# Optimization experiments

Measured on AMD Instinct MI355X. Metric: run time of the kernel, lower is better.

The kernel has to match this reference:

```python
import jax, jax.numpy as jnp
import numpy as np

N, D, H = 2048, 64, 64  # num_nodes, in_channels, hidden_channels


def setup_inputs() -> dict:
    key = jax.random.key(0)
    k0, k1, k2 = jax.random.split(key, 3)
    z = jax.random.normal(k0, (N, D), dtype=jnp.float32)
    # torch.nn.Linear params: W [out, in], y = x @ W.T + b
    W1 = jax.random.normal(k1, (H, 2 * D), dtype=jnp.float32) * (1.0 / np.sqrt(2 * D)).astype(np.float32)
    b1 = jnp.zeros((H,), dtype=jnp.float32)
    W2 = jax.random.normal(k2, (1, H), dtype=jnp.float32) * (1.0 / np.sqrt(H)).astype(np.float32)
    b2 = jnp.zeros((1,), dtype=jnp.float32)
    return {"z": z, "W1": W1, "b1": b1, "W2": W2, "b2": b2}


def reference(z, W1, b1, W2, b2):
    # decode(): adj[i, j] = Linear2(relu(Linear1(cat(z[i], z[j]))))  (dropout off: eval mode)
    # Efficient form: split W1 so cat(z_i, z_j) @ W1.T = z_i @ Wa.T + z_j @ Wb.T,
    # avoiding materializing the [N, N, 2D] concat tensor.
    n, d = z.shape
    Wa, Wb = W1[:, :d], W1[:, d:]           # each [H, D]
    hi = z @ Wa.T                            # [N, H] contribution from row node i
    hj = z @ Wb.T                            # [N, H] contribution from col node j
    h = jax.nn.relu(hi[:, None, :] + hj[None, :, :] + b1)  # [N, N, H]
    adj = jnp.einsum('ijh,h->ij', h, W2[0]) + b2[0]         # [N, N]
    # self_loop_mask=True: zero out the diagonal after sigmoid
    probs = jax.nn.sigmoid(adj) * (1.0 - jnp.eye(n, dtype=adj.dtype))
    return probs
```

## Files before the change

### kernel.cpp

```cpp
#include <hip/hip_runtime.h>
#include <math.h>

#define NN 2048
#define DD 64
#define HH 64

__global__ __launch_bounds__(256) void prep_kernel(
    const float* __restrict__ z, const float* __restrict__ W1,
    const float* __restrict__ b1, const float* __restrict__ W2,
    float* __restrict__ u, float* __restrict__ vt,
    float* __restrict__ a, float* __restrict__ b) {
  __shared__ float zs[8 * DD];
  const int t = threadIdx.x;
  const int i0 = blockIdx.x * 8;
  if (t < 128) {
    reinterpret_cast<float4*>(zs)[t] =
        reinterpret_cast<const float4*>(z + (size_t)i0 * DD)[t];
  }
  __syncthreads();

  const int hs = t & 127;
  const int rg = t >> 7;
  const int h = hs & 63;
  const int side = hs >> 6;
  const float* wrow = W1 + h * (2 * DD) + side * DD;

  float acc0 = 0.f, acc1 = 0.f, acc2 = 0.f, acc3 = 0.f;
#pragma unroll
  for (int d4 = 0; d4 < DD / 4; ++d4) {
    const float4 wv = reinterpret_cast<const float4*>(wrow)[d4];
    const float* z0 = zs + (rg * 4 + 0) * DD + d4 * 4;
    const float* z1 = z0 + DD;
    const float* z2 = z1 + DD;
    const float* z3 = z2 + DD;
    acc0 = fmaf(z0[3], wv.w, fmaf(z0[2], wv.z, fmaf(z0[1], wv.y, fmaf(z0[0], wv.x, acc0))));
    acc1 = fmaf(z1[3], wv.w, fmaf(z1[2], wv.z, fmaf(z1[1], wv.y, fmaf(z1[0], wv.x, acc1))));
    acc2 = fmaf(z2[3], wv.w, fmaf(z2[2], wv.z, fmaf(z2[1], wv.y, fmaf(z2[0], wv.x, acc2))));
    acc3 = fmaf(z3[3], wv.w, fmaf(z3[2], wv.z, fmaf(z3[1], wv.y, fmaf(z3[0], wv.x, acc3))));
  }
  const float bias = side ? 0.0f : b1[h];
  const float s0 = acc0 + bias, s1 = acc1 + bias, s2 = acc2 + bias, s3 = acc3 + bias;
  const int ib = i0 + rg * 4;
  if (side) {
    float* vrow = vt + (size_t)h * NN + ib;
    vrow[0] = s0; vrow[1] = s1; vrow[2] = s2; vrow[3] = s3;
  } else {
    u[(size_t)(ib + 0) * HH + h] = s0;
    u[(size_t)(ib + 1) * HH + h] = s1;
    u[(size_t)(ib + 2) * HH + h] = s2;
    u[(size_t)(ib + 3) * HH + h] = s3;
  }

  const float wh = W2[h];
  float r0 = wh * s0, r1 = wh * s1, r2 = wh * s2, r3 = wh * s3;
#pragma unroll
  for (int m = 1; m < 64; m <<= 1) {
    r0 += __shfl_xor(r0, m);
    r1 += __shfl_xor(r1, m);
    r2 += __shfl_xor(r2, m);
    r3 += __shfl_xor(r3, m);
  }
  if ((t & 63) == 0) {
    float* d2 = side ? b : a;
    d2[ib + 0] = 0.5f * r0;
    d2[ib + 1] = 0.5f * r1;
    d2[ib + 2] = 0.5f * r2;
    d2[ib + 3] = 0.5f * r3;
  }
}

__global__ __launch_bounds__(256, 4) void pair_kernel(
    const float* __restrict__ u, const float* __restrict__ vt,
    const float* __restrict__ a, const float* __restrict__ b,
    const float* __restrict__ W2, const float* __restrict__ b2,
    float* __restrict__ out) {
  const int t = threadIdx.x;
  const int L = t & 63;
  const int w = t >> 6;
  const int i0 = blockIdx.y * 16 + w * 4;
  const int j0 = blockIdx.x * 256;
  const int jL = j0 + 4 * L;

  float ur[4];
#pragma unroll
  for (int m = 0; m < 4; ++m) ur[m] = u[(size_t)(i0 + m) * HH + L];

  const float4* vt4 = reinterpret_cast<const float4*>(vt);
  const int vcol = (j0 >> 2) + L;

  float acc[4][4] = {};
#pragma unroll
  for (int hc = 0; hc < 8; ++hc) {
    float4 q[8];
#pragma unroll
    for (int hh = 0; hh < 8; ++hh)
      q[hh] = vt4[(size_t)(hc * 8 + hh) * (NN / 4) + vcol];
#pragma unroll
    for (int hh = 0; hh < 8; ++hh) {
      const int h = hc * 8 + hh;
      const float wh = W2[h];
#pragma unroll
      for (int m = 0; m < 4; ++m) {
        const float um = __int_as_float(
            __builtin_amdgcn_readlane(__float_as_int(ur[m]), h));
        acc[m][0] = fmaf(wh, fabsf(um + q[hh].x), acc[m][0]);
        acc[m][1] = fmaf(wh, fabsf(um + q[hh].y), acc[m][1]);
        acc[m][2] = fmaf(wh, fabsf(um + q[hh].z), acc[m][2]);
        acc[m][3] = fmaf(wh, fabsf(um + q[hh].w), acc[m][3]);
      }
    }
  }

  const float bias2 = b2[0];
  const float4 bj = *reinterpret_cast<const float4*>(b + jL);
  const float bjv[4] = {bj.x, bj.y, bj.z, bj.w};

#pragma unroll
  for (int m = 0; m < 4; ++m) {
    const int i = i0 + m;
    const float ai = a[i] + bias2;
    float r[4];
#pragma unroll
    for (int c = 0; c < 4; ++c) {
      const float x = ai + bjv[c] + 0.5f * acc[m][c];
      r[c] = 1.0f / (1.0f + __expf(-x));
      if (i == jL + c) r[c] = 0.0f;
    }
    *reinterpret_cast<float4*>(out + (size_t)i * NN + jL) =
        make_float4(r[0], r[1], r[2], r[3]);
  }
}

extern "C" void kernel_launch(void* const* d_in, const int* in_sizes, int n_in,
                              void* d_out, int out_size, void* d_ws, size_t ws_size,
                              hipStream_t stream) {
  const float* z  = (const float*)d_in[0];
  const float* W1 = (const float*)d_in[1];
  const float* b1 = (const float*)d_in[2];
  const float* W2 = (const float*)d_in[3];
  const float* b2 = (const float*)d_in[4];
  float* out = (float*)d_out;

  float* u  = (float*)d_ws;
  float* vt = u + (size_t)NN * HH;
  float* a  = vt + (size_t)NN * HH;
  float* b  = a + NN;

  prep_kernel<<<NN / 8, 256, 0, stream>>>(z, W1, b1, W2, u, vt, a, b);
  pair_kernel<<<dim3(NN / 256, NN / 16), 256, 0, stream>>>(u, vt, a, b, W2, b2, out);
}
```

Baseline: 91.14 us.

## Remap pair kernel so lanes own rows and vt reads become wave-uniform

Reassigns the pair kernel's work so each lane handles one row i and each wave a strip of 8 columns, making vt loads uniform across the wave (scalar-loadable) and removing readlane broadcasts of u. Each lane now loads its own u row with vector loads. Occupancy hint is raised to 8 blocks per SIMD target. The trade-off is strided per-lane u reads and output stores scattered across 64 rows per wave, which may reduce write coalescing.

```diff
diff --git a/kernel.cpp b/kernel.cpp
--- a/kernel.cpp
+++ b/kernel.cpp
@@ -69,7 +69,7 @@
   }
 }
 
-__global__ __launch_bounds__(256, 4) void pair_kernel(
+__global__ __launch_bounds__(256, 8) void pair_kernel(
     const float* __restrict__ u, const float* __restrict__ vt,
     const float* __restrict__ a, const float* __restrict__ b,
     const float* __restrict__ W2, const float* __restrict__ b2,
@@ -77,58 +77,45 @@
   const int t = threadIdx.x;
   const int L = t & 63;
   const int w = t >> 6;
-  const int i0 = blockIdx.y * 16 + w * 4;
-  const int j0 = blockIdx.x * 256;
-  const int jL = j0 + 4 * L;
+  const int i = blockIdx.y * 64 + L;
+  const int j0 = blockIdx.x * 32 + w * 8;
 
-  float ur[4];
+  const float* urow = u + (size_t)i * HH;
+
+  float acc[8] = {};
 #pragma unroll
-  for (int m = 0; m < 4; ++m) ur[m] = u[(size_t)(i0 + m) * HH + L];
-
-  const float4* vt4 = reinterpret_cast<const float4*>(vt);
-  const int vcol = (j0 >> 2) + L;
-
-  float acc[4][4] = {};
+  for (int hc = 0; hc < 4; ++hc) {
+    float u16[16];
 #pragma unroll
-  for (int hc = 0; hc < 8; ++hc) {
-    float4 q[8];
+    for (int q = 0; q < 4; ++q) {
+      const float4 f = *reinterpret_cast<const float4*>(urow + hc * 16 + q * 4);
+      u16[q * 4 + 0] = f.x; u16[q * 4 + 1] = f.y;
+      u16[q * 4 + 2] = f.z; u16[q * 4 + 3] = f.w;
+    }
 #pragma unroll
-    for (int hh = 0; hh < 8; ++hh)
-      q[hh] = vt4[(size_t)(hc * 8 + hh) * (NN / 4) + vcol];
+    for (int hh = 0; hh < 16; ++hh) {
+      const int h = hc * 16 + hh;
+      const float uh = u16[hh];
+      const float wh = W2[h];
+      const float* vr = vt + (size_t)h * NN + j0;
 #pragma unroll
-    for (int hh = 0; hh < 8; ++hh) {
-      const int h = hc * 8 + hh;
-      const float wh = W2[h];
-#pragma unroll
-      for (int m = 0; m < 4; ++m) {
-        const float um = __int_as_float(
-            __builtin_amdgcn_readlane(__float_as_int(ur[m]), h));
-        acc[m][0] = fmaf(wh, fabsf(um + q[hh].x), acc[m][0]);
-        acc[m][1] = fmaf(wh, fabsf(um + q[hh].y), acc[m][1]);
-        acc[m][2] = fmaf(wh, fabsf(um + q[hh].z), acc[m][2]);
-        acc[m][3] = fmaf(wh, fabsf(um + q[hh].w), acc[m][3]);
+      for (int c = 0; c < 8; ++c) {
+        acc[c] = fmaf(wh, fabsf(uh + vr[c]), acc[c]);
       }
     }
   }
 
-  const float bias2 = b2[0];
-  const float4 bj = *reinterpret_cast<const float4*>(b + jL);
-  const float bjv[4] = {bj.x, bj.y, bj.z, bj.w};
-
+  const float ai = a[i] + b2[0];
+  float r[8];
 #pragma unroll
-  for (int m = 0; m < 4; ++m) {
-    const int i = i0 + m;
-    const float ai = a[i] + bias2;
-    float r[4];
-#pragma unroll
-    for (int c = 0; c < 4; ++c) {
-      const float x = ai + bjv[c] + 0.5f * acc[m][c];
-      r[c] = 1.0f / (1.0f + __expf(-x));
-      if (i == jL + c) r[c] = 0.0f;
-    }
-    *reinterpret_cast<float4*>(out + (size_t)i * NN + jL) =
-        make_float4(r[0], r[1], r[2], r[3]);
+  for (int c = 0; c < 8; ++c) {
+    const float x = ai + b[j0 + c] + 0.5f * acc[c];
+    r[c] = 1.0f / (1.0f + __expf(-x));
+    if (i == j0 + c) r[c] = 0.0f;
   }
+  float* orow = out + (size_t)i * NN + j0;
+  *reinterpret_cast<float4*>(orow) = make_float4(r[0], r[1], r[2], r[3]);
+  *reinterpret_cast<float4*>(orow + 4) = make_float4(r[4], r[5], r[6], r[7]);
 }
 
 extern "C" void kernel_launch(void* const* d_in, const int* in_sizes, int n_in,
@@ -147,5 +134,5 @@
   float* b  = a + NN;
 
   prep_kernel<<<NN / 8, 256, 0, stream>>>(z, W1, b1, W2, u, vt, a, b);
-  pair_kernel<<<dim3(NN / 256, NN / 16), 256, 0, stream>>>(u, vt, a, b, W2, b2, out);
+  pair_kernel<<<dim3(NN / 32, NN / 64), 256, 0, stream>>>(u, vt, a, b, W2, b2, out);
 }
```

Measured after the change: 119.2 us. 1.31x slower.
